# Kernel tuning notes

Measured on AMD Instinct MI355X. Metric: run time of the kernel, lower is better.

## Reference

```python
import jax, jax.numpy as jnp
import numpy as np

E = 16        # n_routed_experts
K = 4         # num_experts_per_tok
G = 4         # n_group
TG = 2        # topk_group
NS = 2        # n_shared_experts
H = 1024      # hidden_size
I = 1408      # intermediate_size
SCALE = 1.0   # routed_scaling_factor


def _gate(x2d, gate_w, gate_bias):
    # x2d: [T,H], gate_w: [E,H], gate_bias: [E]
    T = x2d.shape[0]
    logits = x2d.astype(jnp.float32) @ gate_w.astype(jnp.float32).T   # [T,E]
    scores = jax.nn.sigmoid(logits)
    sfc = scores + gate_bias[None, :]
    # group scores = sum of top-2 expert scores within each group
    grp = sfc.reshape(T, G, E // G)
    top2, _ = jax.lax.top_k(grp, 2)
    group_scores = top2.sum(-1)                                       # [T,G]
    _, gidx = jax.lax.top_k(group_scores, TG)                         # [T,TG]
    gmask = jnp.zeros((T, G), sfc.dtype).at[jnp.arange(T)[:, None], gidx].set(1.0)
    smask = jnp.repeat(gmask, E // G, axis=1) > 0                     # [T,E]
    tmp = jnp.where(smask, sfc, 0.0)
    _, topk_idx = jax.lax.top_k(tmp, K)                               # [T,K]
    topk_w = jnp.take_along_axis(scores, topk_idx, axis=1)            # [T,K]
    topk_w = topk_w / (topk_w.sum(-1, keepdims=True) + 1e-20)         # norm_topk_prob
    return topk_idx, topk_w * SCALE


def setup_inputs() -> dict:
    key = jax.random.key(0)
    ks = jax.random.split(key, 8)
    bound = 1.0 / np.sqrt(H)  # kaiming_uniform(a=sqrt(5)) on [E,H]
    return {
        "hidden_states": jax.random.normal(ks[0], (1, 1024, H), jnp.float32),
        "gate_w": jax.random.uniform(ks[1], (E, H), jnp.float32, -bound, bound),
        "gate_bias": jnp.zeros((E,), jnp.float32),
        "gate_proj": jax.random.normal(ks[2], (E, I, H), jnp.float32) * 0.02,
        "up_proj": jax.random.normal(ks[3], (E, I, H), jnp.float32) * 0.02,
        "down_proj": jax.random.normal(ks[4], (E, H, I), jnp.float32) * 0.02,
        "shared_gate_w": jax.random.normal(ks[5], (I * NS, H), jnp.float32) * 0.02,
        "shared_up_w": jax.random.normal(ks[6], (I * NS, H), jnp.float32) * 0.02,
        "shared_down_w": jax.random.normal(ks[7], (H, I * NS), jnp.float32) * 0.02,
    }


def reference(hidden_states, gate_w, gate_bias, gate_proj, up_proj, down_proj,
              shared_gate_w, shared_up_w, shared_down_w):
    orig_shape = hidden_states.shape
    x = hidden_states.reshape(-1, H)                                  # [T,H]
    topk_idx, topk_w = _gate(x, gate_w, gate_bias)
    # per-token per-expert combine weight (top-k indices are unique per token,
    # so scatter-add combine == dense weighted sum)
    combine_w = (jax.nn.one_hot(topk_idx, E, dtype=x.dtype) * topk_w[..., None]).sum(1)  # [T,E]
    g = jnp.einsum('th,eih->tei', x, gate_proj)                       # [T,E,I]
    u = jnp.einsum('th,eih->tei', x, up_proj)
    act = jax.nn.silu(g) * u                                          # SwiGLU
    y = jnp.einsum('tei,ehi,te->th', act, down_proj, combine_w)       # [T,H]
    # shared experts
    sg = x @ shared_gate_w.T
    su = x @ shared_up_w.T
    y = y + (jax.nn.silu(sg) * su) @ shared_down_w.T
    return y.reshape(orig_shape)
```

## Files before the change

kernel.cpp:

```cpp
#include <hip/hip_runtime.h>
#include <hip/hip_bf16.h>

#define T_TOK 1024
#define H_DIM 1024
#define I_DIM 1408
#define NE 16
#define NEP 18
#define BM 256

typedef __attribute__((ext_vector_type(8))) __bf16 bf16x8;
typedef __attribute__((ext_vector_type(4))) float f32x4;

__device__ __forceinline__ bf16x8 cvt8(float4 a, float4 b) {
    bf16x8 r;
    r[0] = (__bf16)a.x; r[1] = (__bf16)a.y; r[2] = (__bf16)a.z; r[3] = (__bf16)a.w;
    r[4] = (__bf16)b.x; r[5] = (__bf16)b.y; r[6] = (__bf16)b.z; r[7] = (__bf16)b.w;
    return r;
}

__device__ __forceinline__ void gll16(const float* g, float* l) {
    __builtin_amdgcn_global_load_lds(
        (const __attribute__((address_space(1))) void*)g,
        (__attribute__((address_space(3))) void*)l, 16, 0, 0);
}

__global__ __launch_bounds__(64) void gate_kernel(
    const float* __restrict__ x, const float* __restrict__ gw,
    const float* __restrict__ gb,
    int* __restrict__ counts, int* __restrict__ etok, float* __restrict__ ew)
{
    const int t = blockIdx.x;
    const int lane = threadIdx.x;
    float s[NE];
#pragma unroll
    for (int e = 0; e < NE; ++e) s[e] = 0.f;
    const float* xr = x + (size_t)t * H_DIM;
    for (int i = lane; i < H_DIM; i += 64) {
        float xv = xr[i];
#pragma unroll
        for (int e = 0; e < NE; ++e) s[e] += xv * gw[e * H_DIM + i];
    }
#pragma unroll
    for (int e = 0; e < NE; ++e) {
        for (int off = 32; off > 0; off >>= 1) s[e] += __shfl_xor(s[e], off);
    }
    if (lane == 0) {
        float scores[NE], sfc[NE];
#pragma unroll
        for (int e = 0; e < NE; ++e) {
            scores[e] = 1.f / (1.f + __expf(-s[e]));
            sfc[e] = scores[e] + gb[e];
        }
        float gsc[4];
#pragma unroll
        for (int g = 0; g < 4; ++g) {
            float m1 = -1e30f, m2 = -1e30f;
#pragma unroll
            for (int j = 0; j < 4; ++j) {
                float v = sfc[4 * g + j];
                if (v > m1) { m2 = m1; m1 = v; } else if (v > m2) { m2 = v; }
            }
            gsc[g] = m1 + m2;
        }
        int g1 = 0;
        for (int g = 1; g < 4; ++g) if (gsc[g] > gsc[g1]) g1 = g;
        int g2 = -1;
        for (int g = 0; g < 4; ++g) {
            if (g == g1) continue;
            if (g2 < 0 || gsc[g] > gsc[g2]) g2 = g;
        }
        float tmp[NE];
#pragma unroll
        for (int e = 0; e < NE; ++e) {
            int gg = e >> 2;
            tmp[e] = (gg == g1 || gg == g2) ? sfc[e] : 0.0f;
        }
        int idxs[4]; float wk[4]; float wsum = 0.f;
#pragma unroll
        for (int k = 0; k < 4; ++k) {
            int bi = 0;
            for (int e = 1; e < NE; ++e) if (tmp[e] > tmp[bi]) bi = e;
            idxs[k] = bi; wk[k] = scores[bi]; wsum += scores[bi];
            tmp[bi] = -1e30f;
        }
        float inv = 1.f / (wsum + 1e-20f);
        for (int k = 0; k < 4; ++k) {
            int e = idxs[k];
            int pos = atomicAdd(&counts[e], 1);
            etok[e * T_TOK + pos] = t;
            ew[e * T_TOK + pos] = wk[k] * inv;
        }
    }
}

__global__ __launch_bounds__(256) void cvtx_kernel(
    const float* __restrict__ x, __hip_bfloat16* __restrict__ x_bf)
{
    int i = (blockIdx.x * 256 + threadIdx.x) * 4;
    float4 v = ((const float4*)x)[i >> 2];
    x_bf[i + 0] = __float2bfloat16(v.x);
    x_bf[i + 1] = __float2bfloat16(v.y);
    x_bf[i + 2] = __float2bfloat16(v.z);
    x_bf[i + 3] = __float2bfloat16(v.w);
}

__global__ __launch_bounds__(256, 2) void gateup_kernel(
    const __hip_bfloat16* __restrict__ x_bf,
    const float* __restrict__ gproj, const float* __restrict__ uproj,
    const float* __restrict__ sgw, const float* __restrict__ suw,
    const int* __restrict__ counts, const int* __restrict__ etok,
    __hip_bfloat16* __restrict__ act, int e0)
{
    const int slot = blockIdx.y;
    const int e = e0 + slot;
    const int cnt = (e < NE) ? counts[e] : T_TOK;
    const int row0 = blockIdx.z * BM;
    if (row0 >= cnt) return;

    __shared__ int toks[BM];
    __shared__ __align__(16) float Bg[2][2048];
    __shared__ __align__(16) float Bu[2][2048];

    const int tid = threadIdx.x;
    {
        int r = row0 + tid;
        toks[tid] = (e < NE) ? ((r < cnt) ? etok[e * T_TOK + r] : 0) : r;
    }

    const int nb0 = blockIdx.x * 64;
    const float *wg, *wu;
    if (e < NE) {
        wg = gproj + (size_t)e * I_DIM * H_DIM;
        wu = uproj + (size_t)e * I_DIM * H_DIM;
    } else {
        wg = sgw + (size_t)(e - NE) * I_DIM * H_DIM;
        wu = suw + (size_t)(e - NE) * I_DIM * H_DIM;
    }

    const int lane = tid & 63;
    const int w = tid >> 6;
    const int col = lane & 15, kq = lane >> 4;

    const int lr8 = lane >> 3;
    const int sgx = (lane & 7) ^ lr8;
    const float* pgW[2]; const float* puW[2];
#pragma unroll
    for (int j = 0; j < 2; ++j) {
        int c = 2 * w + j;
        pgW[j] = wg + (size_t)(nb0 + c * 8 + lr8) * H_DIM + sgx * 4;
        puW[j] = wu + (size_t)(nb0 + c * 8 + lr8) * H_DIM + sgx * 4;
    }

    int offs[4][2];
#pragma unroll
    for (int ni = 0; ni < 4; ++ni) {
        int row = ni * 16 + col;
#pragma unroll
        for (int h = 0; h < 2; ++h)
            offs[ni][h] = row * 32 + (((kq * 2 + h) ^ (row & 7)) << 2);
    }

#pragma unroll
    for (int j = 0; j < 2; ++j) gll16(pgW[j], &Bg[0][(2 * w + j) * 256]);
#pragma unroll
    for (int j = 0; j < 2; ++j) gll16(puW[j], &Bu[0][(2 * w + j) * 256]);
    __syncthreads();

    const __hip_bfloat16* ar[4];
#pragma unroll
    for (int mi = 0; mi < 4; ++mi)
        ar[mi] = x_bf + (size_t)toks[w * 64 + mi * 16 + col] * H_DIM + kq * 8;

    f32x4 accg[4][4], accu[4][4];
#pragma unroll
    for (int mi = 0; mi < 4; ++mi)
#pragma unroll
        for (int ni = 0; ni < 4; ++ni) {
            accg[mi][ni] = (f32x4){0.f, 0.f, 0.f, 0.f};
            accu[mi][ni] = (f32x4){0.f, 0.f, 0.f, 0.f};
        }

    for (int k = 0; k < 32; ++k) {
        const int buf = k & 1;
        asm volatile("s_waitcnt vmcnt(0)" ::: "memory");
        __builtin_amdgcn_s_barrier();
        __builtin_amdgcn_sched_barrier(0);
        bf16x8 a[4];
#pragma unroll
        for (int mi = 0; mi < 4; ++mi) a[mi] = *(const bf16x8*)(ar[mi] + k * 32);
        __builtin_amdgcn_sched_barrier(0);
        if (k + 1 < 32) {
#pragma unroll
            for (int j = 0; j < 2; ++j)
                gll16(pgW[j] + (k + 1) * 32, &Bg[buf ^ 1][(2 * w + j) * 256]);
#pragma unroll
            for (int j = 0; j < 2; ++j)
                gll16(puW[j] + (k + 1) * 32, &Bu[buf ^ 1][(2 * w + j) * 256]);
        }
        __builtin_amdgcn_sched_barrier(0);
        bf16x8 bg[4], bu[4];
#pragma unroll
        for (int ni = 0; ni < 4; ++ni) {
            float4 lo = *(const float4*)&Bg[buf][offs[ni][0]];
            float4 hi = *(const float4*)&Bg[buf][offs[ni][1]];
            bg[ni] = cvt8(lo, hi);
            float4 lo2 = *(const float4*)&Bu[buf][offs[ni][0]];
            float4 hi2 = *(const float4*)&Bu[buf][offs[ni][1]];
            bu[ni] = cvt8(lo2, hi2);
        }
#pragma unroll
        for (int mi = 0; mi < 4; ++mi)
#pragma unroll
            for (int ni = 0; ni < 4; ++ni) {
                accg[mi][ni] = __builtin_amdgcn_mfma_f32_16x16x32_bf16(a[mi], bg[ni], accg[mi][ni], 0, 0, 0);
                accu[mi][ni] = __builtin_amdgcn_mfma_f32_16x16x32_bf16(a[mi], bu[ni], accu[mi][ni], 0, 0, 0);
            }
    }

#pragma unroll
    for (int mi = 0; mi < 4; ++mi)
#pragma unroll
        for (int ni = 0; ni < 4; ++ni)
#pragma unroll
            for (int r = 0; r < 4; ++r) {
                int lrow = w * 64 + mi * 16 + kq * 4 + r;
                int grow = row0 + lrow;
                float g = accg[mi][ni][r];
                float a = (grow < cnt) ? (g / (1.f + __expf(-g)) * accu[mi][ni][r]) : 0.f;
                act[((size_t)slot * T_TOK + grow) * I_DIM + nb0 + ni * 16 + col] =
                    __float2bfloat16(a);
            }
}

__global__ __launch_bounds__(256, 3) void down_kernel(
    const __hip_bfloat16* __restrict__ act,
    const float* __restrict__ dproj, const float* __restrict__ sdw,
    const int* __restrict__ counts, const int* __restrict__ etok,
    const float* __restrict__ ew, float* __restrict__ y, int e0, int ne)
{
    const int hw = blockIdx.x;
    const int c8 = hw & 7, t = hw >> 3;
    const int nbt = t & 15, gh = t >> 4;
    const int g = c8 + 8 * gh;
    if (g >= ne * 4) return;
    const int slot = g % ne;
    const int z = g / ne;

    const int e = e0 + slot;
    const int cnt = (e < NE) ? counts[e] : T_TOK;
    const int row0 = z * BM;
    if (row0 >= cnt) return;

    __shared__ int toks[BM];
    __shared__ float wts[BM];
    __shared__ __align__(16) float Bd[2][2048];

    const int tid = threadIdx.x;
    {
        int r = row0 + tid;
        if (e < NE) {
            bool ok = r < cnt;
            toks[tid] = ok ? etok[e * T_TOK + r] : 0;
            wts[tid]  = ok ? ew[e * T_TOK + r] : 0.f;
        } else { toks[tid] = r; wts[tid] = 1.f; }
    }

    const int nb0 = nbt * 64;
    const float* wd;
    int wstride;
    if (e < NE) { wd = dproj + (size_t)e * H_DIM * I_DIM; wstride = I_DIM; }
    else        { wd = sdw + (size_t)(e - NE) * I_DIM;    wstride = 2 * I_DIM; }

    const int lane = tid & 63;
    const int w = tid >> 6;
    const int col = lane & 15, kq = lane >> 4;

    const int lr8 = lane >> 3;
    const int sgx = (lane & 7) ^ lr8;
    const float* pdW[2];
#pragma unroll
    for (int j = 0; j < 2; ++j) {
        int c = 2 * w + j;
        pdW[j] = wd + (size_t)(nb0 + c * 8 + lr8) * wstride + sgx * 4;
    }

    int offs[4][2];
#pragma unroll
    for (int ni = 0; ni < 4; ++ni) {
        int row = ni * 16 + col;
#pragma unroll
        for (int h = 0; h < 2; ++h)
            offs[ni][h] = row * 32 + (((kq * 2 + h) ^ (row & 7)) << 2);
    }

#pragma unroll
    for (int j = 0; j < 2; ++j) gll16(pdW[j], &Bd[0][(2 * w + j) * 256]);
    __syncthreads();

    const __hip_bfloat16* ar[4];
#pragma unroll
    for (int mi = 0; mi < 4; ++mi)
        ar[mi] = act + ((size_t)slot * T_TOK + row0 + w * 64 + mi * 16 + col) * I_DIM + kq * 8;

    f32x4 acc[4][4];
#pragma unroll
    for (int mi = 0; mi < 4; ++mi)
#pragma unroll
        for (int ni = 0; ni < 4; ++ni) acc[mi][ni] = (f32x4){0.f, 0.f, 0.f, 0.f};

    const int KS = I_DIM / 32;
    for (int k = 0; k < KS; ++k) {
        const int buf = k & 1;
        asm volatile("s_waitcnt vmcnt(0)" ::: "memory");
        __builtin_amdgcn_s_barrier();
        __builtin_amdgcn_sched_barrier(0);
        bf16x8 a[4];
#pragma unroll
        for (int mi = 0; mi < 4; ++mi) a[mi] = *(const bf16x8*)(ar[mi] + k * 32);
        __builtin_amdgcn_sched_barrier(0);
        if (k + 1 < KS) {
#pragma unroll
            for (int j = 0; j < 2; ++j)
                gll16(pdW[j] + (k + 1) * 32, &Bd[buf ^ 1][(2 * w + j) * 256]);
        }
        __builtin_amdgcn_sched_barrier(0);
        bf16x8 b[4];
#pragma unroll
        for (int ni = 0; ni < 4; ++ni) {
            float4 lo = *(const float4*)&Bd[buf][offs[ni][0]];
            float4 hi = *(const float4*)&Bd[buf][offs[ni][1]];
            b[ni] = cvt8(lo, hi);
        }
#pragma unroll
        for (int mi = 0; mi < 4; ++mi)
#pragma unroll
            for (int ni = 0; ni < 4; ++ni)
                acc[mi][ni] = __builtin_amdgcn_mfma_f32_16x16x32_bf16(a[mi], b[ni], acc[mi][ni], 0, 0, 0);
    }

#pragma unroll
    for (int mi = 0; mi < 4; ++mi)
#pragma unroll
        for (int ni = 0; ni < 4; ++ni)
#pragma unroll
            for (int r = 0; r < 4; ++r) {
                int lrow = w * 64 + mi * 16 + kq * 4 + r;
                int grow = row0 + lrow;
                if (grow < cnt)
                    atomicAdd(&y[(size_t)toks[lrow] * H_DIM + nb0 + ni * 16 + col],
                              acc[mi][ni][r] * wts[lrow]);
            }
}

extern "C" void kernel_launch(void* const* d_in, const int* in_sizes, int n_in,
                              void* d_out, int out_size, void* d_ws, size_t ws_size,
                              hipStream_t stream) {
    (void)in_sizes; (void)n_in; (void)out_size;
    const float* x  = (const float*)d_in[0];
    const float* gw = (const float*)d_in[1];
    const float* gb = (const float*)d_in[2];
    const float* gp = (const float*)d_in[3];
    const float* up = (const float*)d_in[4];
    const float* dp = (const float*)d_in[5];
    const float* sg = (const float*)d_in[6];
    const float* su = (const float*)d_in[7];
    const float* sd = (const float*)d_in[8];
    float* out = (float*)d_out;

    char* ws = (char*)d_ws;
    int*   counts = (int*)ws;
    int*   etok   = (int*)(ws + 256);
    float* ew     = (float*)(ws + 256 + 65536);
    __hip_bfloat16* x_bf = (__hip_bfloat16*)(ws + 131328);
    __hip_bfloat16* act  = (__hip_bfloat16*)(ws + 2228480);

    size_t fixed = 2228480;
    size_t per_e = (size_t)T_TOK * I_DIM * 2;
    int cap = NEP;
    if (ws_size < fixed + (size_t)NEP * per_e) {
        cap = (ws_size > fixed + per_e) ? (int)((ws_size - fixed) / per_e) : 1;
        if (cap < 1) cap = 1;
    }

    hipMemsetAsync(ws, 0, 256, stream);
    hipMemsetAsync(out, 0, (size_t)T_TOK * H_DIM * 4, stream);

    gate_kernel<<<dim3(T_TOK), dim3(64), 0, stream>>>(x, gw, gb, counts, etok, ew);
    cvtx_kernel<<<dim3(1024), dim3(256), 0, stream>>>(x, x_bf);

    for (int e0 = 0; e0 < NEP; e0 += cap) {
        int ne = NEP - e0 < cap ? NEP - e0 : cap;
        gateup_kernel<<<dim3(I_DIM / 64, ne, T_TOK / BM), dim3(256), 0, stream>>>(
            x_bf, gp, up, sg, su, counts, etok, act, e0);
        int Gp = ((ne * 4 + 7) / 8) * 8;
        down_kernel<<<dim3(16 * Gp), dim3(256), 0, stream>>>(
            act, dp, sd, counts, etok, ew, out, e0, ne);
    }
}
```

Baseline: 499.5 us.

## Triple-buffer LDS weight tiles and prefetch activation rows one step ahead

```diff
diff --git a/kernel.cpp b/kernel.cpp
--- a/kernel.cpp
+++ b/kernel.cpp
@@ -118,8 +118,8 @@
     if (row0 >= cnt) return;
 
     __shared__ int toks[BM];
-    __shared__ __align__(16) float Bg[2][2048];
-    __shared__ __align__(16) float Bu[2][2048];
+    __shared__ __align__(16) float Bg[3][2048];
+    __shared__ __align__(16) float Bu[3][2048];
 
     const int tid = threadIdx.x;
     {
@@ -150,6 +150,7 @@
         pgW[j] = wg + (size_t)(nb0 + c * 8 + lr8) * H_DIM + sgx * 4;
         puW[j] = wu + (size_t)(nb0 + c * 8 + lr8) * H_DIM + sgx * 4;
     }
+    const int ldsw0 = (2 * w) * 256, ldsw1 = (2 * w + 1) * 256;
 
     int offs[4][2];
 #pragma unroll
@@ -160,10 +161,6 @@
             offs[ni][h] = row * 32 + (((kq * 2 + h) ^ (row & 7)) << 2);
     }
 
-#pragma unroll
-    for (int j = 0; j < 2; ++j) gll16(pgW[j], &Bg[0][(2 * w + j) * 256]);
-#pragma unroll
-    for (int j = 0; j < 2; ++j) gll16(puW[j], &Bu[0][(2 * w + j) * 256]);
     __syncthreads();
 
     const __hip_bfloat16* ar[4];
@@ -180,41 +177,56 @@
             accu[mi][ni] = (f32x4){0.f, 0.f, 0.f, 0.f};
         }
 
+    bf16x8 a_cur[4], a_nxt[4];
+#pragma unroll
+    for (int mi = 0; mi < 4; ++mi) a_cur[mi] = *(const bf16x8*)ar[mi];
+    gll16(pgW[0], &Bg[0][ldsw0]); gll16(pgW[1], &Bg[0][ldsw1]);
+    gll16(puW[0], &Bu[0][ldsw0]); gll16(puW[1], &Bu[0][ldsw1]);
+    gll16(pgW[0] + 32, &Bg[1][ldsw0]); gll16(pgW[1] + 32, &Bg[1][ldsw1]);
+    gll16(puW[0] + 32, &Bu[1][ldsw0]); gll16(puW[1] + 32, &Bu[1][ldsw1]);
+
+    int br = 0;
     for (int k = 0; k < 32; ++k) {
-        const int buf = k & 1;
-        asm volatile("s_waitcnt vmcnt(0)" ::: "memory");
+        asm volatile("s_waitcnt vmcnt(4)" ::: "memory");
         __builtin_amdgcn_s_barrier();
         __builtin_amdgcn_sched_barrier(0);
-        bf16x8 a[4];
-#pragma unroll
-        for (int mi = 0; mi < 4; ++mi) a[mi] = *(const bf16x8*)(ar[mi] + k * 32);
-        __builtin_amdgcn_sched_barrier(0);
         if (k + 1 < 32) {
 #pragma unroll
-            for (int j = 0; j < 2; ++j)
-                gll16(pgW[j] + (k + 1) * 32, &Bg[buf ^ 1][(2 * w + j) * 256]);
-#pragma unroll
-            for (int j = 0; j < 2; ++j)
-                gll16(puW[j] + (k + 1) * 32, &Bu[buf ^ 1][(2 * w + j) * 256]);
-        }
-        __builtin_amdgcn_sched_barrier(0);
+            for (int mi = 0; mi < 4; ++mi)
+                a_nxt[mi] = *(const bf16x8*)(ar[mi] + (k + 1) * 32);
+        }
+        __builtin_amdgcn_sched_barrier(0);
+        if (k + 2 < 32) {
+            int b2 = br + 2; if (b2 >= 3) b2 -= 3;
+            float* bgD = &Bg[0][0] + b2 * 2048;
+            float* buD = &Bu[0][0] + b2 * 2048;
+            const int ko = (k + 2) * 32;
+            gll16(pgW[0] + ko, bgD + ldsw0); gll16(pgW[1] + ko, bgD + ldsw1);
+            gll16(puW[0] + ko, buD + ldsw0); gll16(puW[1] + ko, buD + ldsw1);
+        }
+        __builtin_amdgcn_sched_barrier(0);
+        const float* bgR = &Bg[0][0] + br * 2048;
+        const float* buR = &Bu[0][0] + br * 2048;
         bf16x8 bg[4], bu[4];
 #pragma unroll
         for (int ni = 0; ni < 4; ++ni) {
-            float4 lo = *(const float4*)&Bg[buf][offs[ni][0]];
-            float4 hi = *(const float4*)&Bg[buf][offs[ni][1]];
+            float4 lo = *(const float4*)(bgR + offs[ni][0]);
+            float4 hi = *(const float4*)(bgR + offs[ni][1]);
             bg[ni] = cvt8(lo, hi);
-            float4 lo2 = *(const float4*)&Bu[buf][offs[ni][0]];
-            float4 hi2 = *(const float4*)&Bu[buf][offs[ni][1]];
+            float4 lo2 = *(const float4*)(buR + offs[ni][0]);
+            float4 hi2 = *(const float4*)(buR + offs[ni][1]);
             bu[ni] = cvt8(lo2, hi2);
         }
 #pragma unroll
         for (int mi = 0; mi < 4; ++mi)
 #pragma unroll
             for (int ni = 0; ni < 4; ++ni) {
-                accg[mi][ni] = __builtin_amdgcn_mfma_f32_16x16x32_bf16(a[mi], bg[ni], accg[mi][ni], 0, 0, 0);
-                accu[mi][ni] = __builtin_amdgcn_mfma_f32_16x16x32_bf16(a[mi], bu[ni], accu[mi][ni], 0, 0, 0);
+                accg[mi][ni] = __builtin_amdgcn_mfma_f32_16x16x32_bf16(a_cur[mi], bg[ni], accg[mi][ni], 0, 0, 0);
+                accu[mi][ni] = __builtin_amdgcn_mfma_f32_16x16x32_bf16(a_cur[mi], bu[ni], accu[mi][ni], 0, 0, 0);
             }
+#pragma unroll
+        for (int mi = 0; mi < 4; ++mi) a_cur[mi] = a_nxt[mi];
+        br += 1; if (br >= 3) br = 0;
     }
 
 #pragma unroll
@@ -253,7 +265,7 @@
 
     __shared__ int toks[BM];
     __shared__ float wts[BM];
-    __shared__ __align__(16) float Bd[2][2048];
+    __shared__ __align__(16) float Bd[3][2048];
 
     const int tid = threadIdx.x;
     {
@@ -283,6 +295,7 @@
         int c = 2 * w + j;
         pdW[j] = wd + (size_t)(nb0 + c * 8 + lr8) * wstride + sgx * 4;
     }
+    const int ldsw0 = (2 * w) * 256, ldsw1 = (2 * w + 1) * 256;
 
     int offs[4][2];
 #pragma unroll
@@ -293,8 +306,6 @@
             offs[ni][h] = row * 32 + (((kq * 2 + h) ^ (row & 7)) << 2);
     }
 
-#pragma unroll
-    for (int j = 0; j < 2; ++j) gll16(pdW[j], &Bd[0][(2 * w + j) * 256]);
     __syncthreads();
 
     const __hip_bfloat16* ar[4];
@@ -309,33 +320,46 @@
         for (int ni = 0; ni < 4; ++ni) acc[mi][ni] = (f32x4){0.f, 0.f, 0.f, 0.f};
 
     const int KS = I_DIM / 32;
+    bf16x8 a_cur[4], a_nxt[4];
+#pragma unroll
+    for (int mi = 0; mi < 4; ++mi) a_cur[mi] = *(const bf16x8*)ar[mi];
+    gll16(pdW[0], &Bd[0][ldsw0]); gll16(pdW[1], &Bd[0][ldsw1]);
+    gll16(pdW[0] + 32, &Bd[1][ldsw0]); gll16(pdW[1] + 32, &Bd[1][ldsw1]);
+
+    int br = 0;
     for (int k = 0; k < KS; ++k) {
-        const int buf = k & 1;
-        asm volatile("s_waitcnt vmcnt(0)" ::: "memory");
+        asm volatile("s_waitcnt vmcnt(2)" ::: "memory");
         __builtin_amdgcn_s_barrier();
         __builtin_amdgcn_sched_barrier(0);
-        bf16x8 a[4];
-#pragma unroll
-        for (int mi = 0; mi < 4; ++mi) a[mi] = *(const bf16x8*)(ar[mi] + k * 32);
-        __builtin_amdgcn_sched_barrier(0);
         if (k + 1 < KS) {
 #pragma unroll
-            for (int j = 0; j < 2; ++j)
-                gll16(pdW[j] + (k + 1) * 32, &Bd[buf ^ 1][(2 * w + j) * 256]);
-        }
-        __builtin_amdgcn_sched_barrier(0);
+            for (int mi = 0; mi < 4; ++mi)
+                a_nxt[mi] = *(const bf16x8*)(ar[mi] + (k + 1) * 32);
+        }
+        __builtin_amdgcn_sched_barrier(0);
+        if (k + 2 < KS) {
+            int b2 = br + 2; if (b2 >= 3) b2 -= 3;
+            float* bdD = &Bd[0][0] + b2 * 2048;
+            const int ko = (k + 2) * 32;
+            gll16(pdW[0] + ko, bdD + ldsw0); gll16(pdW[1] + ko, bdD + ldsw1);
+        }
+        __builtin_amdgcn_sched_barrier(0);
+        const float* bdR = &Bd[0][0] + br * 2048;
         bf16x8 b[4];
 #pragma unroll
         for (int ni = 0; ni < 4; ++ni) {
-            float4 lo = *(const float4*)&Bd[buf][offs[ni][0]];
-            float4 hi = *(const float4*)&Bd[buf][offs[ni][1]];
+            float4 lo = *(const float4*)(bdR + offs[ni][0]);
+            float4 hi = *(const float4*)(bdR + offs[ni][1]);
             b[ni] = cvt8(lo, hi);
         }
 #pragma unroll
         for (int mi = 0; mi < 4; ++mi)
 #pragma unroll
             for (int ni = 0; ni < 4; ++ni)
-                acc[mi][ni] = __builtin_amdgcn_mfma_f32_16x16x32_bf16(a[mi], b[ni], acc[mi][ni], 0, 0, 0);
+                acc[mi][ni] = __builtin_amdgcn_mfma_f32_16x16x32_bf16(a_cur[mi], b[ni], acc[mi][ni], 0, 0, 0);
+#pragma unroll
+        for (int mi = 0; mi < 4; ++mi) a_cur[mi] = a_nxt[mi];
+        br += 1; if (br >= 3) br = 0;
     }
 
 #pragma unroll
```

After: 488.8 us. -2.2%, faster.

## Deepen gate-up and down GEMM pipelines to four-stage buffering, widen gate kernel

Applied to the files above, without the earlier changes.

```diff
diff --git a/kernel.cpp b/kernel.cpp
--- a/kernel.cpp
+++ b/kernel.cpp
@@ -24,18 +24,23 @@
         (__attribute__((address_space(3))) void*)l, 16, 0, 0);
 }
 
-__global__ __launch_bounds__(64) void gate_kernel(
+__global__ __launch_bounds__(256) void gate_kernel(
     const float* __restrict__ x, const float* __restrict__ gw,
     const float* __restrict__ gb,
     int* __restrict__ counts, int* __restrict__ etok, float* __restrict__ ew)
 {
     const int t = blockIdx.x;
-    const int lane = threadIdx.x;
+    const int tid = threadIdx.x;
+    const int lane = tid & 63, w = tid >> 6;
+    __shared__ float red[4][NE];
+
     float s[NE];
 #pragma unroll
     for (int e = 0; e < NE; ++e) s[e] = 0.f;
     const float* xr = x + (size_t)t * H_DIM;
-    for (int i = lane; i < H_DIM; i += 64) {
+#pragma unroll
+    for (int j = 0; j < 4; ++j) {
+        int i = tid + j * 256;
         float xv = xr[i];
 #pragma unroll
         for (int e = 0; e < NE; ++e) s[e] += xv * gw[e * H_DIM + i];
@@ -45,10 +50,16 @@
         for (int off = 32; off > 0; off >>= 1) s[e] += __shfl_xor(s[e], off);
     }
     if (lane == 0) {
+#pragma unroll
+        for (int e = 0; e < NE; ++e) red[w][e] = s[e];
+    }
+    __syncthreads();
+    if (tid == 0) {
         float scores[NE], sfc[NE];
 #pragma unroll
         for (int e = 0; e < NE; ++e) {
-            scores[e] = 1.f / (1.f + __expf(-s[e]));
+            float lg = red[0][e] + red[1][e] + red[2][e] + red[3][e];
+            scores[e] = 1.f / (1.f + __expf(-lg));
             sfc[e] = scores[e] + gb[e];
         }
         float gsc[4];
@@ -118,8 +129,8 @@
     if (row0 >= cnt) return;
 
     __shared__ int toks[BM];
-    __shared__ __align__(16) float Bg[2][2048];
-    __shared__ __align__(16) float Bu[2][2048];
+    __shared__ __align__(16) float Bg[4][2048];
+    __shared__ __align__(16) float Bu[4][2048];
 
     const int tid = threadIdx.x;
     {
@@ -150,6 +161,7 @@
         pgW[j] = wg + (size_t)(nb0 + c * 8 + lr8) * H_DIM + sgx * 4;
         puW[j] = wu + (size_t)(nb0 + c * 8 + lr8) * H_DIM + sgx * 4;
     }
+    const int ldsw0 = (2 * w) * 256, ldsw1 = (2 * w + 1) * 256;
 
     int offs[4][2];
 #pragma unroll
@@ -160,10 +172,6 @@
             offs[ni][h] = row * 32 + (((kq * 2 + h) ^ (row & 7)) << 2);
     }
 
-#pragma unroll
-    for (int j = 0; j < 2; ++j) gll16(pgW[j], &Bg[0][(2 * w + j) * 256]);
-#pragma unroll
-    for (int j = 0; j < 2; ++j) gll16(puW[j], &Bu[0][(2 * w + j) * 256]);
     __syncthreads();
 
     const __hip_bfloat16* ar[4];
@@ -180,42 +188,87 @@
             accu[mi][ni] = (f32x4){0.f, 0.f, 0.f, 0.f};
         }
 
-    for (int k = 0; k < 32; ++k) {
-        const int buf = k & 1;
-        asm volatile("s_waitcnt vmcnt(0)" ::: "memory");
+    bf16x8 a[4][4];
+
+#pragma unroll
+    for (int p = 0; p < 3; ++p) {
+#pragma unroll
+        for (int mi = 0; mi < 4; ++mi)
+            a[p][mi] = *(const bf16x8*)(ar[mi] + p * 32);
+        gll16(pgW[0] + p * 32, &Bg[p][ldsw0]);
+        gll16(pgW[1] + p * 32, &Bg[p][ldsw1]);
+        gll16(puW[0] + p * 32, &Bu[p][ldsw0]);
+        gll16(puW[1] + p * 32, &Bu[p][ldsw1]);
+    }
+
+#define GU_COMPUTE(KK)                                                         \
+    {                                                                          \
+        const float* bgR = &Bg[(KK)][0];                                       \
+        const float* buR = &Bu[(KK)][0];                                       \
+        bf16x8 bg[4], bu[4];                                                   \
+        _Pragma("unroll")                                                      \
+        for (int ni = 0; ni < 4; ++ni) {                                       \
+            float4 lo = *(const float4*)(bgR + offs[ni][0]);                   \
+            float4 hi = *(const float4*)(bgR + offs[ni][1]);                   \
+            bg[ni] = cvt8(lo, hi);                                             \
+            float4 lo2 = *(const float4*)(buR + offs[ni][0]);                  \
+            float4 hi2 = *(const float4*)(buR + offs[ni][1]);                  \
+            bu[ni] = cvt8(lo2, hi2);                                           \
+        }                                                                      \
+        _Pragma("unroll")                                                      \
+        for (int mi = 0; mi < 4; ++mi)                                         \
+            _Pragma("unroll")                                                  \
+            for (int ni = 0; ni < 4; ++ni) {                                   \
+                accg[mi][ni] = __builtin_amdgcn_mfma_f32_16x16x32_bf16(        \
+                    a[(KK)][mi], bg[ni], accg[mi][ni], 0, 0, 0);               \
+                accu[mi][ni] = __builtin_amdgcn_mfma_f32_16x16x32_bf16(        \
+                    a[(KK)][mi], bu[ni], accu[mi][ni], 0, 0, 0);               \
+            }                                                                  \
+    }
+
+    for (int kt = 0; kt < 7; ++kt) {
+#pragma unroll
+        for (int kk = 0; kk < 4; ++kk) {
+            const int k = kt * 4 + kk;
+            asm volatile("s_waitcnt vmcnt(16)" ::: "memory");
+            __builtin_amdgcn_s_barrier();
+            __builtin_amdgcn_sched_barrier(0);
+            {
+                const int kp = k + 3, bp = (kk + 3) & 3;
+#pragma unroll
+                for (int mi = 0; mi < 4; ++mi)
+                    a[bp][mi] = *(const bf16x8*)(ar[mi] + kp * 32);
+                const int ko = kp * 32;
+                gll16(pgW[0] + ko, &Bg[bp][ldsw0]);
+                gll16(pgW[1] + ko, &Bg[bp][ldsw1]);
+                gll16(puW[0] + ko, &Bu[bp][ldsw0]);
+                gll16(puW[1] + ko, &Bu[bp][ldsw1]);
+            }
+            __builtin_amdgcn_sched_barrier(0);
+            GU_COMPUTE(kk);
+        }
+    }
+#pragma unroll
+    for (int kk = 0; kk < 4; ++kk) {
+        if (kk == 0)      asm volatile("s_waitcnt vmcnt(16)" ::: "memory");
+        else if (kk == 1) asm volatile("s_waitcnt vmcnt(16)" ::: "memory");
+        else if (kk == 2) asm volatile("s_waitcnt vmcnt(8)" ::: "memory");
+        else              asm volatile("s_waitcnt vmcnt(0)" ::: "memory");
         __builtin_amdgcn_s_barrier();
         __builtin_amdgcn_sched_barrier(0);
-        bf16x8 a[4];
-#pragma unroll
-        for (int mi = 0; mi < 4; ++mi) a[mi] = *(const bf16x8*)(ar[mi] + k * 32);
+        if (kk == 0) {
+#pragma unroll
+            for (int mi = 0; mi < 4; ++mi)
+                a[3][mi] = *(const bf16x8*)(ar[mi] + 31 * 32);
+            gll16(pgW[0] + 31 * 32, &Bg[3][ldsw0]);
+            gll16(pgW[1] + 31 * 32, &Bg[3][ldsw1]);
+            gll16(puW[0] + 31 * 32, &Bu[3][ldsw0]);
+            gll16(puW[1] + 31 * 32, &Bu[3][ldsw1]);
+        }
         __builtin_amdgcn_sched_barrier(0);
-        if (k + 1 < 32) {
-#pragma unroll
-            for (int j = 0; j < 2; ++j)
-                gll16(pgW[j] + (k + 1) * 32, &Bg[buf ^ 1][(2 * w + j) * 256]);
-#pragma unroll
-            for (int j = 0; j < 2; ++j)
-                gll16(puW[j] + (k + 1) * 32, &Bu[buf ^ 1][(2 * w + j) * 256]);
-        }
-        __builtin_amdgcn_sched_barrier(0);
-        bf16x8 bg[4], bu[4];
-#pragma unroll
-        for (int ni = 0; ni < 4; ++ni) {
-            float4 lo = *(const float4*)&Bg[buf][offs[ni][0]];
-            float4 hi = *(const float4*)&Bg[buf][offs[ni][1]];
-            bg[ni] = cvt8(lo, hi);
-            float4 lo2 = *(const float4*)&Bu[buf][offs[ni][0]];
-            float4 hi2 = *(const float4*)&Bu[buf][offs[ni][1]];
-            bu[ni] = cvt8(lo2, hi2);
-        }
-#pragma unroll
-        for (int mi = 0; mi < 4; ++mi)
-#pragma unroll
-            for (int ni = 0; ni < 4; ++ni) {
-                accg[mi][ni] = __builtin_amdgcn_mfma_f32_16x16x32_bf16(a[mi], bg[ni], accg[mi][ni], 0, 0, 0);
-                accu[mi][ni] = __builtin_amdgcn_mfma_f32_16x16x32_bf16(a[mi], bu[ni], accu[mi][ni], 0, 0, 0);
-            }
-    }
+        GU_COMPUTE(kk);
+    }
+#undef GU_COMPUTE
 
 #pragma unroll
     for (int mi = 0; mi < 4; ++mi)
@@ -226,9 +279,9 @@
                 int lrow = w * 64 + mi * 16 + kq * 4 + r;
                 int grow = row0 + lrow;
                 float g = accg[mi][ni][r];
-                float a = (grow < cnt) ? (g / (1.f + __expf(-g)) * accu[mi][ni][r]) : 0.f;
+                float a2 = (grow < cnt) ? (g / (1.f + __expf(-g)) * accu[mi][ni][r]) : 0.f;
                 act[((size_t)slot * T_TOK + grow) * I_DIM + nb0 + ni * 16 + col] =
-                    __float2bfloat16(a);
+                    __float2bfloat16(a2);
             }
 }
 
@@ -253,7 +306,7 @@
 
     __shared__ int toks[BM];
     __shared__ float wts[BM];
-    __shared__ __align__(16) float Bd[2][2048];
+    __shared__ __align__(16) float Bd[4][2048];
 
     const int tid = threadIdx.x;
     {
@@ -283,6 +336,7 @@
         int c = 2 * w + j;
         pdW[j] = wd + (size_t)(nb0 + c * 8 + lr8) * wstride + sgx * 4;
     }
+    const int ldsw0 = (2 * w) * 256, ldsw1 = (2 * w + 1) * 256;
 
     int offs[4][2];
 #pragma unroll
@@ -293,8 +347,6 @@
             offs[ni][h] = row * 32 + (((kq * 2 + h) ^ (row & 7)) << 2);
     }
 
-#pragma unroll
-    for (int j = 0; j < 2; ++j) gll16(pdW[j], &Bd[0][(2 * w + j) * 256]);
     __syncthreads();
 
     const __hip_bfloat16* ar[4];
@@ -308,35 +360,74 @@
 #pragma unroll
         for (int ni = 0; ni < 4; ++ni) acc[mi][ni] = (f32x4){0.f, 0.f, 0.f, 0.f};
 
+    bf16x8 a[4][4];
+#pragma unroll
+    for (int p = 0; p < 3; ++p) {
+#pragma unroll
+        for (int mi = 0; mi < 4; ++mi)
+            a[p][mi] = *(const bf16x8*)(ar[mi] + p * 32);
+        gll16(pdW[0] + p * 32, &Bd[p][ldsw0]);
+        gll16(pdW[1] + p * 32, &Bd[p][ldsw1]);
+    }
+
+#define D_COMPUTE(KK)                                                          \
+    {                                                                          \
+        const float* bdR = &Bd[(KK)][0];                                       \
+        bf16x8 b[4];                                                           \
+        _Pragma("unroll")                                                      \
+        for (int ni = 0; ni < 4; ++ni) {                                       \
+            float4 lo = *(const float4*)(bdR + offs[ni][0]);                   \
+            float4 hi = *(const float4*)(bdR + offs[ni][1]);                   \
+            b[ni] = cvt8(lo, hi);                                              \
+        }                                                                      \
+        _Pragma("unroll")                                                      \
+        for (int mi = 0; mi < 4; ++mi)                                         \
+            _Pragma("unroll")                                                  \
+            for (int ni = 0; ni < 4; ++ni)                                     \
+                acc[mi][ni] = __builtin_amdgcn_mfma_f32_16x16x32_bf16(         \
+                    a[(KK)][mi], b[ni], acc[mi][ni], 0, 0, 0);                 \
+    }
+
     const int KS = I_DIM / 32;
-    for (int k = 0; k < KS; ++k) {
-        const int buf = k & 1;
-        asm volatile("s_waitcnt vmcnt(0)" ::: "memory");
+    for (int kt = 0; kt < 10; ++kt) {
+#pragma unroll
+        for (int kk = 0; kk < 4; ++kk) {
+            const int k = kt * 4 + kk;
+            asm volatile("s_waitcnt vmcnt(12)" ::: "memory");
+            __builtin_amdgcn_s_barrier();
+            __builtin_amdgcn_sched_barrier(0);
+            {
+                const int kp = k + 3, bp = (kk + 3) & 3;
+#pragma unroll
+                for (int mi = 0; mi < 4; ++mi)
+                    a[bp][mi] = *(const bf16x8*)(ar[mi] + kp * 32);
+                gll16(pdW[0] + kp * 32, &Bd[bp][ldsw0]);
+                gll16(pdW[1] + kp * 32, &Bd[bp][ldsw1]);
+            }
+            __builtin_amdgcn_sched_barrier(0);
+            D_COMPUTE(kk);
+        }
+    }
+#pragma unroll
+    for (int kk = 0; kk < 4; ++kk) {
+        if (kk == 0)      asm volatile("s_waitcnt vmcnt(12)" ::: "memory");
+        else if (kk == 1) asm volatile("s_waitcnt vmcnt(12)" ::: "memory");
+        else if (kk == 2) asm volatile("s_waitcnt vmcnt(6)" ::: "memory");
+        else              asm volatile("s_waitcnt vmcnt(0)" ::: "memory");
         __builtin_amdgcn_s_barrier();
         __builtin_amdgcn_sched_barrier(0);
-        bf16x8 a[4];
-#pragma unroll
-        for (int mi = 0; mi < 4; ++mi) a[mi] = *(const bf16x8*)(ar[mi] + k * 32);
+        if (kk == 0) {
+#pragma unroll
+            for (int mi = 0; mi < 4; ++mi)
+                a[3][mi] = *(const bf16x8*)(ar[mi] + 43 * 32);
+            gll16(pdW[0] + 43 * 32, &Bd[3][ldsw0]);
+            gll16(pdW[1] + 43 * 32, &Bd[3][ldsw1]);
+        }
         __builtin_amdgcn_sched_barrier(0);
-        if (k + 1 < KS) {
-#pragma unroll
-            for (int j = 0; j < 2; ++j)
-                gll16(pdW[j] + (k + 1) * 32, &Bd[buf ^ 1][(2 * w + j) * 256]);
-        }
-        __builtin_amdgcn_sched_barrier(0);
-        bf16x8 b[4];
-#pragma unroll
-        for (int ni = 0; ni < 4; ++ni) {
-            float4 lo = *(const float4*)&Bd[buf][offs[ni][0]];
-            float4 hi = *(const float4*)&Bd[buf][offs[ni][1]];
-            b[ni] = cvt8(lo, hi);
-        }
-#pragma unroll
-        for (int mi = 0; mi < 4; ++mi)
-#pragma unroll
-            for (int ni = 0; ni < 4; ++ni)
-                acc[mi][ni] = __builtin_amdgcn_mfma_f32_16x16x32_bf16(a[mi], b[ni], acc[mi][ni], 0, 0, 0);
-    }
+        D_COMPUTE(kk);
+    }
+#undef D_COMPUTE
+    (void)KS;
 
 #pragma unroll
     for (int mi = 0; mi < 4; ++mi)
@@ -385,7 +476,7 @@
     hipMemsetAsync(ws, 0, 256, stream);
     hipMemsetAsync(out, 0, (size_t)T_TOK * H_DIM * 4, stream);
 
-    gate_kernel<<<dim3(T_TOK), dim3(64), 0, stream>>>(x, gw, gb, counts, etok, ew);
+    gate_kernel<<<dim3(T_TOK), dim3(256), 0, stream>>>(x, gw, gb, counts, etok, ew);
     cvtx_kernel<<<dim3(1024), dim3(256), 0, stream>>>(x, x_bf);
 
     for (int e0 = 0; e0 < NEP; e0 += cap) {
```

New measurement: 673.1 us. 34.7% more time.
